# Kernel tuning notes

Hardware: AMD Instinct MI355X
Metric: run time of the kernel (lower is better)

## Reference

```python
import jax, jax.numpy as jnp
import numpy as np

B, N = 4096, 8192
A = 0.5                      # activation stretch
G = 0.7853981633974483       # entanglement angle (pi/4)
SIN_G = np.sin(G)
PI = np.pi


def setup_inputs() -> dict:
    key = jax.random.key(0)
    k1, k2, k3 = jax.random.split(key, 3)
    inp = jax.random.normal(k1, (B, N), dtype=jnp.float32)
    angles = 0.1 * jax.random.normal(k2, (B, N), dtype=jnp.float32)
    # previous measurement results are +/-1
    last_res = jnp.sign(jax.random.normal(k3, (B, N), dtype=jnp.float32))
    last_res = jnp.where(last_res == 0, 1.0, last_res)
    return {"input": inp, "angles": angles, "last_res": last_res}


def reference(input, angles, last_res):
    # rotation angle from activation (a != 0 branch: tanh(input/a))
    thetas = (PI / 2) * (last_res - jnp.tanh(input / A))
    temp_angles = angles + thetas
    betas = jnp.sin(temp_angles / 2)                       # [B, N]
    exp_z = jnp.cos(temp_angles / 2) ** 2 - betas ** 2     # = cos(temp_angles)
    exp_z_anc = exp_z * SIN_G
    # two-outcome categorical (Bernoulli) with clamped probs
    p0 = jnp.clip((1 + exp_z_anc) / 2, 0.0, None)          # outcome +1
    p1 = jnp.clip((1 - exp_z_anc) / 2, 0.0, None)          # outcome -1
    u = jax.random.uniform(jax.random.key(42), input.shape, dtype=input.dtype)
    meas_res = jnp.where(u < p0 / (p0 + p1), 1.0, -1.0).astype(input.dtype)
    # post-measurement state update
    side = betas * jnp.sqrt((1 - meas_res * SIN_G) / (1 + meas_res * exp_z_anc))
    side = jnp.clip(side, -1.0, 1.0)
    new_angles = 2 * jnp.arcsin(side)
    # torch module updates angles<-new_angles, last_res<-meas_res in-place and
    # returns meas_res; we return the updated state explicitly.
    return meas_res, new_angles
```

## Files before the change

### kernel.cpp

```cpp
#include <hip/hip_runtime.h>
#include <cstdint>

#pragma clang fp contract(off)

__device__ __forceinline__ uint32_t rotl32(uint32_t x, uint32_t r) {
  return (x << r) | (x >> (32u - r));
}

__device__ __forceinline__ uint32_t threefry_bits(uint32_t idx) {
  const uint32_t ks0 = 0u;
  const uint32_t ks1 = 42u;
  const uint32_t ks2 = 0x1BD11BDAu ^ 0u ^ 42u;
  uint32_t x0 = 0u + ks0;
  uint32_t x1 = idx + ks1;
#define TF_R(r) { x0 += x1; x1 = rotl32(x1, r); x1 ^= x0; }
  TF_R(13u) TF_R(15u) TF_R(26u) TF_R(6u)
  x0 += ks1; x1 += ks2 + 1u;
  TF_R(17u) TF_R(29u) TF_R(16u) TF_R(24u)
  x0 += ks2; x1 += ks0 + 2u;
  TF_R(13u) TF_R(15u) TF_R(26u) TF_R(6u)
  x0 += ks0; x1 += ks1 + 3u;
  TF_R(17u) TF_R(29u) TF_R(16u) TF_R(24u)
  x0 += ks1; x1 += ks2 + 4u;
  TF_R(13u) TF_R(15u) TF_R(26u) TF_R(6u)
  x0 += ks2; x1 += ks0 + 5u;
#undef TF_R
  return x0 ^ x1;
}

__device__ __forceinline__ float xla_fast_tanh(float x) {
  const float kClamp = 7.90531110763549805f;
  float abs_x = fabsf(x);
  float xc = fminf(fmaxf(x, -kClamp), kClamp);
  float x2 = xc * xc;
  float num = -2.76076847742355e-16f;
  num = num * x2; num = num + 2.00018790482477e-13f;
  num = num * x2; num = num + -8.60467152213735e-11f;
  num = num * x2; num = num + 5.12229709037114e-08f;
  num = num * x2; num = num + 1.48572235717979e-05f;
  num = num * x2; num = num + 6.37261928875436e-04f;
  num = num * x2; num = num + 4.89352455891786e-03f;
  num = xc * num;
  float den = 1.19825839466702e-06f;
  den = den * x2; den = den + 1.18534705686654e-04f;
  den = den * x2; den = den + 2.26843463243900e-03f;
  den = den * x2; den = den + 4.89352518554385e-03f;
  float r = num / den;
  return (abs_x < 0.0004f) ? x : r;
}

__device__ __forceinline__ void compute_one(float in_v, float ang_v, float lr_v,
                                            uint32_t idx, float& meas,
                                            float& nang) {
  const float kHalfPi = 1.5707963267948966f;
  const float kSinG   = 0.7071067811865476f;

  float t = xla_fast_tanh(in_v * 2.0f);
  float theta = kHalfPi * (lr_v - t);
  float temp = ang_v + theta;
  float h = temp * 0.5f;
  float be = sinf(h);
  float co = cosf(h);
  float exp_z = (co * co) - (be * be);
  float e = exp_z * kSinG;
  float p0 = fmaxf((1.0f + e) * 0.5f, 0.0f);
  float p1 = fmaxf((1.0f - e) * 0.5f, 0.0f);
  float ratio = p0 / (p0 + p1);

  uint32_t bits = threefry_bits(idx);
  float u = __uint_as_float((bits >> 9) | 0x3f800000u) - 1.0f;
  float m = (u < ratio) ? 1.0f : -1.0f;

  float numr = 1.0f - m * kSinG;
  float denr = 1.0f + m * e;
  float side = be * sqrtf(numr / denr);
  side = fminf(fmaxf(side, -1.0f), 1.0f);

  float ss = side * side;
  float at = atan2f(side, 1.0f + sqrtf(1.0f - ss));
  nang = 2.0f * (2.0f * at);
  meas = m;
}

__global__ __launch_bounds__(256) void wmeasure_kernel(
    const float4* __restrict__ inp, const float4* __restrict__ ang,
    const float4* __restrict__ lres, float* __restrict__ out,
    int n4, int n) {
#pragma clang fp contract(off)
  int i = blockIdx.x * blockDim.x + threadIdx.x;
  if (i >= n4) return;

  float4 vi = inp[i];
  float4 va = ang[i];
  float4 vl = lres[i];

  const float* pi_ = reinterpret_cast<const float*>(&vi);
  const float* pa_ = reinterpret_cast<const float*>(&va);
  const float* pl_ = reinterpret_cast<const float*>(&vl);

  float4 vm, vn;
  float* pm_ = reinterpret_cast<float*>(&vm);
  float* pn_ = reinterpret_cast<float*>(&vn);

  uint32_t base = ((uint32_t)i) << 2;
#pragma unroll
  for (int j = 0; j < 4; ++j) {
    compute_one(pi_[j], pa_[j], pl_[j], base + (uint32_t)j, pm_[j], pn_[j]);
  }

  reinterpret_cast<float4*>(out)[i] = vm;
  reinterpret_cast<float4*>(out + n)[i] = vn;
}

extern "C" void kernel_launch(void* const* d_in, const int* in_sizes, int n_in,
                              void* d_out, int out_size, void* d_ws,
                              size_t ws_size, hipStream_t stream) {
  const float* inp = (const float*)d_in[0];
  const float* ang = (const float*)d_in[1];
  const float* lr  = (const float*)d_in[2];
  float* out = (float*)d_out;

  int n = in_sizes[0];
  int n4 = n >> 2;
  int blocks = (n4 + 255) / 256;

  wmeasure_kernel<<<blocks, 256, 0, stream>>>(
      (const float4*)inp, (const float4*)ang, (const float4*)lr, out, n4, n);
}
```

Measured before the change: 552.7 us.

## Vectorize elementwise math and replace atan2/sqrt with fast polynomial asin tail

Rewrites the per-element compute on 4-wide vector types. It uses alignbit for the threefry rotations and fused sincosf instead of separate sin/cos calls. It replaces the atan2f-based arcsin with a half-angle reduction built on hardware sqrt/rcp and a minimax atan polynomial, and it simplifies the post-measurement ratio with selects. The aim is to cut ALU instruction count in a kernel where math-heavy work may dominate, at the cost of small deviations in accuracy from the hardware approximations and the polynomial.

```diff
diff --git a/kernel.cpp b/kernel.cpp
--- a/kernel.cpp
+++ b/kernel.cpp
@@ -3,8 +3,11 @@
 
 #pragma clang fp contract(off)
 
+typedef float    f32x4 __attribute__((ext_vector_type(4)));
+typedef uint32_t u32x4 __attribute__((ext_vector_type(4)));
+
 __device__ __forceinline__ uint32_t rotl32(uint32_t x, uint32_t r) {
-  return (x << r) | (x >> (32u - r));
+  return __builtin_amdgcn_alignbit(x, x, 32u - r);
 }
 
 __device__ __forceinline__ uint32_t threefry_bits(uint32_t idx) {
@@ -28,12 +31,11 @@
   return x0 ^ x1;
 }
 
-__device__ __forceinline__ float xla_fast_tanh(float x) {
-  const float kClamp = 7.90531110763549805f;
-  float abs_x = fabsf(x);
-  float xc = fminf(fmaxf(x, -kClamp), kClamp);
-  float x2 = xc * xc;
-  float num = -2.76076847742355e-16f;
+__device__ __forceinline__ f32x4 xla_fast_tanh_v4(f32x4 x) {
+  const f32x4 kC = (f32x4)7.90531110763549805f;
+  f32x4 xc = __builtin_elementwise_min(__builtin_elementwise_max(x, -kC), kC);
+  f32x4 x2 = xc * xc;
+  f32x4 num = (f32x4)(-2.76076847742355e-16f);
   num = num * x2; num = num + 2.00018790482477e-13f;
   num = num * x2; num = num + -8.60467152213735e-11f;
   num = num * x2; num = num + 5.12229709037114e-08f;
@@ -41,89 +43,115 @@
   num = num * x2; num = num + 6.37261928875436e-04f;
   num = num * x2; num = num + 4.89352455891786e-03f;
   num = xc * num;
-  float den = 1.19825839466702e-06f;
+  f32x4 den = (f32x4)1.19825839466702e-06f;
   den = den * x2; den = den + 1.18534705686654e-04f;
   den = den * x2; den = den + 2.26843463243900e-03f;
   den = den * x2; den = den + 4.89352518554385e-03f;
-  float r = num / den;
-  return (abs_x < 0.0004f) ? x : r;
+  f32x4 r = num / den;
+  f32x4 out;
+#pragma unroll
+  for (int j = 0; j < 4; ++j)
+    out[j] = (fabsf(x[j]) < 0.0004f) ? x[j] : r[j];
+  return out;
 }
 
-__device__ __forceinline__ void compute_one(float in_v, float ang_v, float lr_v,
-                                            uint32_t idx, float& meas,
-                                            float& nang) {
+__device__ __forceinline__ f32x4 asin_tail_v4(f32x4 side) {
+#pragma clang fp contract(fast)
+  f32x4 ss = side * side;
+  f32x4 om = 1.0f - ss;
+  f32x4 sq, s;
+#pragma unroll
+  for (int j = 0; j < 4; ++j) sq[j] = __builtin_amdgcn_sqrtf(om[j]);
+  f32x4 d = 1.0f + sq;
+#pragma unroll
+  for (int j = 0; j < 4; ++j) s[j] = side[j] * __builtin_amdgcn_rcpf(d[j]);
+  f32x4 t2 = s * s;
+  f32x4 r = (f32x4)(-4.0540580e-3f);
+  r = r * t2 + 2.18612288e-2f;
+  r = r * t2 + -5.59098861e-2f;
+  r = r * t2 + 9.64200441e-2f;
+  r = r * t2 + -1.390853351e-1f;
+  r = r * t2 + 1.994653599e-1f;
+  r = r * t2 + -3.332985605e-1f;
+  r = r * t2 + 9.999993329e-1f;
+  return 4.0f * (s * r);
+}
+
+__global__ __launch_bounds__(256) void wmeasure_kernel(
+    const f32x4* __restrict__ inp, const f32x4* __restrict__ ang,
+    const f32x4* __restrict__ lres, float* __restrict__ out,
+    int n4, int n) {
+#pragma clang fp contract(off)
   const float kHalfPi = 1.5707963267948966f;
   const float kSinG   = 0.7071067811865476f;
 
-  float t = xla_fast_tanh(in_v * 2.0f);
-  float theta = kHalfPi * (lr_v - t);
-  float temp = ang_v + theta;
-  float h = temp * 0.5f;
-  float be = sinf(h);
-  float co = cosf(h);
-  float exp_z = (co * co) - (be * be);
-  float e = exp_z * kSinG;
-  float p0 = fmaxf((1.0f + e) * 0.5f, 0.0f);
-  float p1 = fmaxf((1.0f - e) * 0.5f, 0.0f);
-  float ratio = p0 / (p0 + p1);
-
-  uint32_t bits = threefry_bits(idx);
-  float u = __uint_as_float((bits >> 9) | 0x3f800000u) - 1.0f;
-  float m = (u < ratio) ? 1.0f : -1.0f;
-
-  float numr = 1.0f - m * kSinG;
-  float denr = 1.0f + m * e;
-  float side = be * sqrtf(numr / denr);
-  side = fminf(fmaxf(side, -1.0f), 1.0f);
-
-  float ss = side * side;
-  float at = atan2f(side, 1.0f + sqrtf(1.0f - ss));
-  nang = 2.0f * (2.0f * at);
-  meas = m;
-}
-
-__global__ __launch_bounds__(256) void wmeasure_kernel(
-    const float4* __restrict__ inp, const float4* __restrict__ ang,
-    const float4* __restrict__ lres, float* __restrict__ out,
-    int n4, int n) {
-#pragma clang fp contract(off)
   int i = blockIdx.x * blockDim.x + threadIdx.x;
   if (i >= n4) return;
 
-  float4 vi = inp[i];
-  float4 va = ang[i];
-  float4 vl = lres[i];
+  f32x4 vi = inp[i];
+  f32x4 va = ang[i];
+  f32x4 vl = lres[i];
 
-  const float* pi_ = reinterpret_cast<const float*>(&vi);
-  const float* pa_ = reinterpret_cast<const float*>(&va);
-  const float* pl_ = reinterpret_cast<const float*>(&vl);
-
-  float4 vm, vn;
-  float* pm_ = reinterpret_cast<float*>(&vm);
-  float* pn_ = reinterpret_cast<float*>(&vn);
-
-  uint32_t base = ((uint32_t)i) << 2;
+  f32x4 t = xla_fast_tanh_v4(vi * 2.0f);
+  f32x4 theta = kHalfPi * (vl - t);
+  f32x4 temp = va + theta;
+  f32x4 h = temp * 0.5f;
+  f32x4 be, co;
 #pragma unroll
   for (int j = 0; j < 4; ++j) {
-    compute_one(pi_[j], pa_[j], pl_[j], base + (uint32_t)j, pm_[j], pn_[j]);
+    float sj, cj;
+    sincosf(h[j], &sj, &cj);
+    be[j] = sj; co[j] = cj;
   }
+  f32x4 exp_z = (co * co) - (be * be);
+  f32x4 e = exp_z * kSinG;
+  f32x4 onepe = 1.0f + e;
+  f32x4 oneme = 1.0f - e;
+  f32x4 p0 = __builtin_elementwise_max(onepe * 0.5f, (f32x4)0.0f);
+  f32x4 p1 = __builtin_elementwise_max(oneme * 0.5f, (f32x4)0.0f);
+  f32x4 ratio = p0 / (p0 + p1);
 
-  reinterpret_cast<float4*>(out)[i] = vm;
-  reinterpret_cast<float4*>(out + n)[i] = vn;
+  u32x4 bits;
+  uint32_t basei = ((uint32_t)i) << 2;
+#pragma unroll
+  for (int j = 0; j < 4; ++j) bits[j] = threefry_bits(basei + (uint32_t)j);
+  u32x4 ub = (bits >> 9) | 0x3f800000u;
+  f32x4 v = __builtin_bit_cast(f32x4, ub);
+  f32x4 u = v - 1.0f;
+
+  f32x4 m, numr, denr;
+#pragma unroll
+  for (int j = 0; j < 4; ++j) {
+    bool pos = u[j] < ratio[j];
+    m[j]    = pos ? 1.0f : -1.0f;
+    numr[j] = pos ? (1.0f - kSinG) : (1.0f + kSinG);
+    denr[j] = pos ? onepe[j] : oneme[j];
+  }
+  f32x4 q = numr / denr;
+  f32x4 sq;
+#pragma unroll
+  for (int j = 0; j < 4; ++j) sq[j] = sqrtf(q[j]);
+  f32x4 side = be * sq;
+  side = __builtin_elementwise_min(
+             __builtin_elementwise_max(side, (f32x4)(-1.0f)), (f32x4)1.0f);
+
+  f32x4 nang = asin_tail_v4(side);
+
+  reinterpret_cast<f32x4*>(out)[i] = m;
+  reinterpret_cast<f32x4*>(out + n)[i] = nang;
 }
 
 extern "C" void kernel_launch(void* const* d_in, const int* in_sizes, int n_in,
                               void* d_out, int out_size, void* d_ws,
                               size_t ws_size, hipStream_t stream) {
-  const float* inp = (const float*)d_in[0];
-  const float* ang = (const float*)d_in[1];
-  const float* lr  = (const float*)d_in[2];
+  const f32x4* inp = (const f32x4*)d_in[0];
+  const f32x4* ang = (const f32x4*)d_in[1];
+  const f32x4* lr  = (const f32x4*)d_in[2];
   float* out = (float*)d_out;
 
   int n = in_sizes[0];
   int n4 = n >> 2;
   int blocks = (n4 + 255) / 256;
 
-  wmeasure_kernel<<<blocks, 256, 0, stream>>>(
-      (const float4*)inp, (const float4*)ang, (const float4*)lr, out, n4, n);
+  wmeasure_kernel<<<blocks, 256, 0, stream>>>(inp, ang, lr, out, n4, n);
 }
```

Result: faster. 532.5 us (-3.7%).
